# Kernel optimization log

Measured on AMD Instinct MI355X. Metric: run time of the kernel, lower is better.

Reference implementation:

```python
import jax, jax.numpy as jnp
import numpy as np

N_HEADS = 8
WINDOW = 4
KS = 3
N_LAYERS = 6
EPS = 1e-5


def _rel_to_abs(x):
    # x: [B,H,L,2L-1] relative logits -> [B,H,L,L] absolute
    b, h, l, _ = x.shape
    x = jnp.pad(x, ((0, 0), (0, 0), (0, 0), (0, 1)))
    x = x.reshape(b, h, l * 2 * l)
    x = jnp.pad(x, ((0, 0), (0, 0), (0, l - 1)))
    return x.reshape(b, h, l + 1, 2 * l - 1)[:, :, :l, l - 1:]


def _abs_to_rel(x):
    # x: [B,H,L,L] -> [B,H,L,2L-1]
    b, h, l, _ = x.shape
    x = jnp.pad(x, ((0, 0), (0, 0), (0, 0), (0, l - 1)))
    x = x.reshape(b, h, l * (2 * l - 1))
    x = jnp.pad(x, ((0, 0), (0, 0), (l, 0)))
    return x.reshape(b, h, l, 2 * l)[:, :, :, 1:]


def _get_rel_emb(emb, t):
    # emb: [2*WINDOW+1, D] -> [2t-1, D]
    pad = max(t - (WINDOW + 1), 0)
    start = max((WINDOW + 1) - t, 0)
    emb = jnp.pad(emb, ((pad, pad), (0, 0)))
    return emb[start:start + 2 * t - 1]


def _layer_norm(x, g, b):
    # normalize over channel dim (axis 1) of [B,C,T]
    m = jnp.mean(x, axis=1, keepdims=True)
    v = jnp.mean((x - m) ** 2, axis=1, keepdims=True)
    return (x - m) * jax.lax.rsqrt(v + EPS) * g[None, :, None] + b[None, :, None]


def _attn(x, w, bvec, erk, erv, attn_mask):
    # x: [B,C,T]; w: [4,C,C] (q,k,v,o 1x1 convs); bvec: [4,C]
    B, C, T = x.shape
    kch = C // N_HEADS

    def proj(i):
        h = jnp.einsum('oc,bct->bot', w[i], x) + bvec[i][None, :, None]
        return h.reshape(B, N_HEADS, kch, T).transpose(0, 1, 3, 2)  # [B,H,T,D]

    q, k, v = proj(0), proj(1), proj(2)
    scale = np.float32(1.0 / np.sqrt(kch))
    scores = jnp.einsum('bhtd,bhsd->bhts', q * scale, k)
    kr = _get_rel_emb(erk, T)  # [2T-1, D]
    scores = scores + _rel_to_abs(jnp.einsum('bhtd,md->bhtm', q * scale, kr))
    scores = jnp.where(attn_mask == 0, jnp.float32(-1e4), scores)
    p = jax.nn.softmax(scores, axis=-1)
    out = jnp.einsum('bhts,bhsd->bhtd', p, v)
    vr = _get_rel_emb(erv, T)
    out = out + jnp.einsum('bhtm,md->bhtd', _abs_to_rel(p), vr)
    out = out.transpose(0, 1, 3, 2).reshape(B, C, T)
    return jnp.einsum('oc,bct->bot', w[3], out) + bvec[3][None, :, None]


def _conv1d_same(h, wt, bt):
    pad_l, pad_r = (KS - 1) // 2, KS // 2
    hp = jnp.pad(h, ((0, 0), (0, 0), (pad_l, pad_r)))
    y = jax.lax.conv_general_dilated(hp, wt, (1,), 'VALID',
                                     dimension_numbers=('NCH', 'OIH', 'NCH'))
    return y + bt[None, :, None]


def _ffn(x, mask, w1, b1, w2, b2):
    h = jax.nn.relu(_conv1d_same(x * mask, w1, b1))  # activation=None -> relu
    return _conv1d_same(h * mask, w2, b2) * mask


def reference(x, x_mask, attn_w, attn_b, erk, erv, ln1_g, ln1_b,
              ffn_w1, ffn_b1, ffn_w2, ffn_b2, ln2_g, ln2_b):
    attn_mask = x_mask[:, :, :, None] * x_mask[:, :, None, :]  # [B,1,T,T]
    x = x * x_mask
    for i in range(N_LAYERS):
        y = _attn(x, attn_w[i], attn_b[i], erk[i], erv[i], attn_mask)
        x = _layer_norm(x + y, ln1_g[i], ln1_b[i])
        y = _ffn(x, x_mask, ffn_w1[i], ffn_b1[i], ffn_w2[i], ffn_b2[i])
        x = _layer_norm(x + y, ln2_g[i], ln2_b[i])
    return x * x_mask


def setup_inputs() -> dict:
    B, C, T, F, L = 8, 512, 1024, 2048, N_LAYERS
    kch = C // N_HEADS
    key = jax.random.key(0)
    ks = jax.random.split(key, 8)
    std = 0.02
    return {
        'x': jax.random.normal(ks[0], (B, C, T), jnp.float32),
        'x_mask': jnp.ones((B, 1, T), jnp.float32),
        'attn_w': jax.random.normal(ks[1], (L, 4, C, C), jnp.float32) * std,
        'attn_b': jnp.zeros((L, 4, C), jnp.float32),
        'erk': jax.random.normal(ks[2], (L, 2 * WINDOW + 1, kch), jnp.float32) * (kch ** -0.5),
        'erv': jax.random.normal(ks[3], (L, 2 * WINDOW + 1, kch), jnp.float32) * (kch ** -0.5),
        'ln1_g': jnp.ones((L, C), jnp.float32),
        'ln1_b': jnp.zeros((L, C), jnp.float32),
        'ffn_w1': jax.random.normal(ks[4], (L, F, C, KS), jnp.float32) * std,
        'ffn_b1': jnp.zeros((L, F), jnp.float32),
        'ffn_w2': jax.random.normal(ks[5], (L, C, F, KS), jnp.float32) * std,
        'ffn_b2': jnp.zeros((L, C), jnp.float32),
        'ln2_g': jnp.ones((L, C), jnp.float32),
        'ln2_b': jnp.zeros((L, C), jnp.float32),
    }
```

## Files before the change

### kernel.cpp

```cpp
#include <hip/hip_runtime.h>

typedef __bf16 bf16_t;
typedef __bf16 bf16x8 __attribute__((ext_vector_type(8)));
typedef __bf16 bf16x4 __attribute__((ext_vector_type(4)));
typedef float  f32x4  __attribute__((ext_vector_type(4)));

#define AS1 __attribute__((address_space(1)))
#define AS3 __attribute__((address_space(3)))

#define CMAX 16.0f

template<int BM, int BN, int OUTMN, int CONV, int BIAS, int RELU, int MASK>
__global__ __launch_bounds__(256)
void gemm_nt(const bf16_t* __restrict__ A, const bf16_t* __restrict__ B,
             bf16_t* __restrict__ C, const float* __restrict__ bias,
             const float* __restrict__ mask, const bf16_t* __restrict__ zpage,
             int K, int lda, int ldb, int ldc, int CIN,
             long sAb, long sAh, long sBb, long sBh, long sCb, long sCh)
{
    constexpr int BK = 32;
    __shared__ bf16_t As[BM * BK];
    __shared__ bf16_t Bs[BN * BK];
    const int z = blockIdx.z;
    int tap0 = 0;
    if constexpr (CONV == 2) {
        tap0 = z;
        A += (long)tap0 * CIN;
    } else {
        A += (long)(z >> 3) * sAb + (long)(z & 7) * sAh;
        B += (long)(z >> 3) * sBb + (long)(z & 7) * sBh;
        C += (long)(z >> 3) * sCb + (long)(z & 7) * sCh;
    }
    const int m0 = blockIdx.y * BM;
    const int n0 = blockIdx.x * BN;
    const int tid = threadIdx.x;
    const int wid = tid >> 6, lane = tid & 63;
    constexpr int WM = BM / 2, WN = BN / 2;
    constexpr int FM = WM / 16, FN = WN / 16;
    const int wm = wid >> 1, wn = wid & 1;

    f32x4 acc[FM][FN] = {};

    constexpr int ACH = BM / 64;
    constexpr int BCH = BN / 64;
    const int rquad = lane >> 2;
    const int koff  = (lane & 3) * 8;

    int tap = 0, cc0 = 0;
    for (int k0 = 0; k0 < K; k0 += BK) {
        #pragma unroll
        for (int q = 0; q < ACH; ++q) {
            int ch  = wid * ACH + q;
            int row = ch * 16 + rquad;
            const bf16_t* src = A + (long)(m0 + row) * lda + (k0 + koff);
            __builtin_amdgcn_global_load_lds((const AS1 void*)src,
                                             (AS3 void*)(As + ch * 512), 16, 0, 0);
        }
        #pragma unroll
        for (int q = 0; q < BCH; ++q) {
            int ch  = wid * BCH + q;
            int row = ch * 16 + rquad;
            const bf16_t* src;
            if constexpr (CONV == 1) {
                int tl = (n0 & 1023) + row + tap - 1;
                src = ((unsigned)tl < 1024u)
                    ? B + (long)(n0 + row + tap - 1) * ldb + (cc0 + koff)
                    : zpage + koff;
            } else if constexpr (CONV == 2) {
                int tl = (n0 & 1023) + row + tap0 - 1;
                src = ((unsigned)tl < 1024u)
                    ? B + (long)(n0 + row + tap0 - 1) * ldb + (k0 + koff)
                    : zpage + koff;
            } else {
                src = B + (long)(n0 + row) * ldb + (k0 + koff);
            }
            __builtin_amdgcn_global_load_lds((const AS1 void*)src,
                                             (AS3 void*)(Bs + ch * 512), 16, 0, 0);
        }
        if constexpr (CONV == 1) { cc0 += BK; if (cc0 == CIN) { cc0 = 0; ++tap; } }
        __syncthreads();

        const bf16_t* Ab = As + (wm * WM + (lane & 15)) * BK + ((lane >> 4) * 8);
        const bf16_t* Bb = Bs + (wn * WN + (lane & 15)) * BK + ((lane >> 4) * 8);
        bf16x8 af[FM], bv[FN];
        #pragma unroll
        for (int i = 0; i < FM; ++i) af[i] = *(const bf16x8*)(Ab + i * 16 * BK);
        #pragma unroll
        for (int j = 0; j < FN; ++j) bv[j] = *(const bf16x8*)(Bb + j * 16 * BK);
        #pragma unroll
        for (int i = 0; i < FM; ++i)
            #pragma unroll
            for (int j = 0; j < FN; ++j)
                acc[i][j] = __builtin_amdgcn_mfma_f32_16x16x32_bf16(af[i], bv[j], acc[i][j], 0, 0, 0);
        __syncthreads();
    }

    const int mw = m0 + wm * WM, nw = n0 + wn * WN;
    #pragma unroll
    for (int i = 0; i < FM; ++i) {
        const int mb = mw + i * 16 + (lane >> 4) * 4;
        f32x4 bvv = {};
        if constexpr (BIAS) bvv = *(const f32x4*)(bias + mb);
        #pragma unroll
        for (int j = 0; j < FN; ++j) {
            const int nn = nw + j * 16 + (lane & 15);
            f32x4 v = acc[i][j];
            if constexpr (BIAS) v += bvv;
            if constexpr (RELU) {
                #pragma unroll
                for (int r = 0; r < 4; ++r) v[r] = fmaxf(v[r], 0.f);
            }
            if constexpr (MASK) v *= mask[nn];
            bf16x4 o;
            #pragma unroll
            for (int r = 0; r < 4; ++r) o[r] = (bf16_t)v[r];
            if constexpr (CONV == 2) {
                *(bf16x4*)(C + ((long)tap0 << 22) + (long)nn * 512 + mb) = o;
            } else if constexpr (OUTMN) {
                #pragma unroll
                for (int r = 0; r < 4; ++r) C[(long)(mb + r) * ldc + nn] = (bf16_t)v[r];
            } else {
                *(bf16x4*)(C + (long)nn * ldc + mb) = o;
            }
        }
    }
}

__global__ __launch_bounds__(256)
void rel_qk(const bf16_t* __restrict__ qk, const float* __restrict__ erk_l,
            float* __restrict__ R)
{
    int gw = blockIdx.x * 4 + (threadIdx.x >> 6);
    int z = gw >> 10, t = gw & 1023;
    int b = z >> 3, h = z & 7;
    int lane = threadIdx.x & 63;
    float qv = (float)qk[(long)(b * 1024 + t) * 1024 + h * 64 + lane];
    float r[9];
    #pragma unroll
    for (int j = 0; j < 9; ++j) r[j] = qv * erk_l[j * 64 + lane];
    #pragma unroll
    for (int o = 1; o < 64; o <<= 1)
        #pragma unroll
        for (int j = 0; j < 9; ++j) r[j] += __shfl_xor(r[j], o);
    if (lane == 0) {
        #pragma unroll
        for (int j = 0; j < 9; ++j) R[(long)gw * 9 + j] = r[j];
    }
}

__global__ __launch_bounds__(256)
void mask_bias(const float* __restrict__ mask, float* __restrict__ kb)
{
    int i = blockIdx.x * 256 + threadIdx.x;
    if (i < 8192) kb[i] = (mask[i] == 0.f) ? -1e4f : 0.f;
}

__global__ __launch_bounds__(256)
void flash_attn(const bf16_t* __restrict__ qk, const bf16_t* __restrict__ vt,
                const float* __restrict__ R, const float* __restrict__ kb,
                bf16_t* __restrict__ out, float* __restrict__ stats)
{
    __shared__ bf16_t P_lds[4 * 1024];
    const int w = threadIdx.x >> 6, lane = threadIdx.x & 63;
    const int hi = lane >> 4, li = lane & 15;
    const int bh = blockIdx.x, b = bh >> 3, h = bh & 7;
    const int q0 = blockIdx.y * 64 + w * 16;
    const long nbase = (long)b * 1024;
    char* pw = (char*)(P_lds + w * 1024);

    const bf16_t* qrow = qk + (nbase + q0 + li) * 1024 + h * 64 + hi * 8;
    bf16x8 aq0 = *(const bf16x8*)(qrow);
    bf16x8 aq1 = *(const bf16x8*)(qrow + 32);

    bf16x8 ones;
    #pragma unroll
    for (int e = 0; e < 8; ++e) ones[e] = (bf16_t)1.0f;

    f32x4 acc_o[4] = {};
    f32x4 acc_l = {};

    const bf16_t* kbase = qk + nbase * 1024 + 512 + h * 64 + hi * 8;
    const bf16_t* vbase = vt + (long)(h * 64 + li) * 8192 + nbase + hi * 8;
    const float* kbp = kb + b * 1024;

    bf16x8 kc[4][2], vv[4][2];
    #pragma unroll
    for (int j = 0; j < 4; ++j) {
        const bf16_t* kr = kbase + (long)(j * 16 + li) * 1024;
        kc[j][0] = *(const bf16x8*)kr;
        kc[j][1] = *(const bf16x8*)(kr + 32);
    }

    for (int it = 0; it < 16; ++it) {
        const int s0 = it * 64;
        #pragma unroll
        for (int j2 = 0; j2 < 4; ++j2) {
            const bf16_t* vr = vbase + (long)(j2 * 16) * 8192 + s0;
            vv[j2][0] = *(const bf16x8*)vr;
            vv[j2][1] = *(const bf16x8*)(vr + 32);
        }
        float kbv[4];
        #pragma unroll
        for (int j = 0; j < 4; ++j) kbv[j] = kbp[s0 + j * 16 + li];
        f32x4 sc[4];
        __builtin_amdgcn_s_setprio(1);
        #pragma unroll
        for (int j = 0; j < 4; ++j) {
            f32x4 a = {};
            a = __builtin_amdgcn_mfma_f32_16x16x32_bf16(aq0, kc[j][0], a, 0, 0, 0);
            a = __builtin_amdgcn_mfma_f32_16x16x32_bf16(aq1, kc[j][1], a, 0, 0, 0);
            sc[j] = a;
        }
        __builtin_amdgcn_s_setprio(0);
        const int s1 = (s0 + 64) & 1023;
        #pragma unroll
        for (int j = 0; j < 4; ++j) {
            const bf16_t* kr = kbase + (long)(s1 + j * 16 + li) * 1024;
            kc[j][0] = *(const bf16x8*)kr;
            kc[j][1] = *(const bf16x8*)(kr + 32);
        }
        #pragma unroll
        for (int j = 0; j < 4; ++j) {
            const int sb = s0 + j * 16;
            const bool near = (sb + 15 >= q0 - 4) && (sb <= q0 + 19);
            const int s_abs = sb + li;
            #pragma unroll
            for (int r = 0; r < 4; ++r) {
                const int q_abs = q0 + hi * 4 + r;
                float v = sc[j][r] + kbv[j];
                if (near) {
                    int jb = s_abs - q_abs + 4;
                    if ((unsigned)jb < 9u)
                        v += R[((long)bh * 1024 + q_abs) * 9 + jb];
                }
                sc[j][r] = __expf(v - CMAX);
            }
        }
        #pragma unroll
        for (int j = 0; j < 4; ++j)
            #pragma unroll
            for (int r = 0; r < 4; ++r) {
                int q = hi * 4 + r;
                int c = (j * 32 + li * 2) ^ ((q & 7) << 4);
                *(bf16_t*)(pw + q * 128 + c) = (bf16_t)sc[j][r];
            }
        asm volatile("s_waitcnt lgkmcnt(0)" ::: "memory");
        __builtin_amdgcn_s_setprio(1);
        #pragma unroll
        for (int half = 0; half < 2; ++half) {
            int cr = (half * 64 + hi * 16) ^ ((li & 7) << 4);
            bf16x8 pa = *(const bf16x8*)(pw + li * 128 + cr);
            #pragma unroll
            for (int j2 = 0; j2 < 4; ++j2)
                acc_o[j2] = __builtin_amdgcn_mfma_f32_16x16x32_bf16(pa, vv[j2][half], acc_o[j2], 0, 0, 0);
            acc_l = __builtin_amdgcn_mfma_f32_16x16x32_bf16(pa, ones, acc_l, 0, 0, 0);
        }
        __builtin_amdgcn_s_setprio(0);
    }

    #pragma unroll
    for (int r = 0; r < 4; ++r) {
        const float inv = 1.f / acc_l[r];
        const int q_abs = q0 + hi * 4 + r;
        #pragma unroll
        for (int j2 = 0; j2 < 4; ++j2) {
            const int d = j2 * 16 + li;
            out[(nbase + q_abs) * 512 + h * 64 + d] = (bf16_t)(acc_o[j2][r] * inv);
        }
        if (li == 0) {
            stats[2 * ((long)bh * 1024 + q_abs)]     = CMAX;
            stats[2 * ((long)bh * 1024 + q_abs) + 1] = acc_l[r];
        }
    }
}

__global__ __launch_bounds__(256)
void band_finish(const bf16_t* __restrict__ qk, const float* __restrict__ R,
                 const float* __restrict__ stats, const float* __restrict__ erv_l,
                 const float* __restrict__ kb, bf16_t* __restrict__ out)
{
    int gw = blockIdx.x * 4 + (threadIdx.x >> 6);
    int bh = gw >> 10, t = gw & 1023;
    int b = bh >> 3, h = bh & 7;
    int lane = threadIdx.x & 63;
    const long nb = (long)b * 1024;
    float qv = (float)qk[(nb + t) * 1024 + h * 64 + lane];
    float p[9];
    #pragma unroll
    for (int j = 0; j < 9; ++j) {
        int s = t + j - 4;
        float dot = 0.f;
        if ((unsigned)s < 1024u)
            dot = qv * (float)qk[(nb + s) * 1024 + 512 + h * 64 + lane];
        p[j] = dot;
    }
    #pragma unroll
    for (int o = 1; o < 64; o <<= 1)
        #pragma unroll
        for (int j = 0; j < 9; ++j) p[j] += __shfl_xor(p[j], o);
    float m = stats[2 * (long)gw], invl = 1.f / stats[2 * (long)gw + 1];
    #pragma unroll
    for (int j = 0; j < 9; ++j) {
        int s = t + j - 4;
        if ((unsigned)s < 1024u) {
            float sc = p[j] + R[(long)gw * 9 + j] + kb[b * 1024 + s];
            p[j] = __expf(sc - m) * invl;
        } else p[j] = 0.f;
    }
    long oidx = (nb + t) * 512 + h * 64 + lane;
    float v = (float)out[oidx];
    #pragma unroll
    for (int j = 0; j < 9; ++j) v += p[j] * erv_l[j * 64 + lane];
    out[oidx] = (bf16_t)v;
}

template<int MASKOUT>
__global__ __launch_bounds__(256)
void ln_residual(float* __restrict__ xres, const bf16_t* __restrict__ y,
                 bf16_t* __restrict__ xbf, const float* __restrict__ g,
                 const float* __restrict__ bvec, const float* __restrict__ mask)
{
    int gw = blockIdx.x * 4 + (threadIdx.x >> 6);
    int lane = threadIdx.x & 63;
    long base = (long)gw * 512 + lane * 8;
    f32x4 x0 = *(const f32x4*)(xres + base);
    f32x4 x1 = *(const f32x4*)(xres + base + 4);
    bf16x8 yv = *(const bf16x8*)(y + base);
    float s[8];
    #pragma unroll
    for (int e = 0; e < 4; ++e) { s[e] = x0[e] + (float)yv[e]; s[4 + e] = x1[e] + (float)yv[4 + e]; }
    float sum = 0.f, sq = 0.f;
    #pragma unroll
    for (int e = 0; e < 8; ++e) { sum += s[e]; sq += s[e] * s[e]; }
    #pragma unroll
    for (int o = 1; o < 64; o <<= 1) { sum += __shfl_xor(sum, o); sq += __shfl_xor(sq, o); }
    float mean = sum * (1.f / 512.f);
    float var  = sq * (1.f / 512.f) - mean * mean;
    float rstd = rsqrtf(var + 1e-5f);
    f32x4 g0 = *(const f32x4*)(g + lane * 8);
    f32x4 g1 = *(const f32x4*)(g + lane * 8 + 4);
    f32x4 b0 = *(const f32x4*)(bvec + lane * 8);
    f32x4 b1 = *(const f32x4*)(bvec + lane * 8 + 4);
    float mk = MASKOUT ? mask[gw] : 1.f;
    f32x4 o0, o1; bf16x8 ob;
    #pragma unroll
    for (int e = 0; e < 4; ++e) {
        float v0 = (s[e] - mean) * rstd * g0[e] + b0[e];
        float v1 = (s[4 + e] - mean) * rstd * g1[e] + b1[e];
        o0[e] = v0; o1[e] = v1;
        ob[e] = (bf16_t)(v0 * mk); ob[4 + e] = (bf16_t)(v1 * mk);
    }
    *(f32x4*)(xres + base) = o0;
    *(f32x4*)(xres + base + 4) = o1;
    *(bf16x8*)(xbf + base) = ob;
}

__global__ __launch_bounds__(256)
void ln_residual_p3(float* __restrict__ xres, const bf16_t* __restrict__ part,
                    bf16_t* __restrict__ xbf, const float* __restrict__ g,
                    const float* __restrict__ bvec, const float* __restrict__ bias,
                    const float* __restrict__ mask)
{
    int gw = blockIdx.x * 4 + (threadIdx.x >> 6);
    int lane = threadIdx.x & 63;
    long base = (long)gw * 512 + lane * 8;
    bf16x8 pa = *(const bf16x8*)(part + base);
    bf16x8 pbv = *(const bf16x8*)(part + base + (1l << 22));
    bf16x8 pc = *(const bf16x8*)(part + base + (2l << 22));
    f32x4 x0 = *(const f32x4*)(xres + base);
    f32x4 x1 = *(const f32x4*)(xres + base + 4);
    f32x4 bi0 = *(const f32x4*)(bias + lane * 8);
    f32x4 bi1 = *(const f32x4*)(bias + lane * 8 + 4);
    float mk = mask[gw];
    float s[8];
    #pragma unroll
    for (int e = 0; e < 4; ++e) {
        float y0 = ((float)pa[e] + (float)pbv[e] + (float)pc[e] + bi0[e]) * mk;
        float y1 = ((float)pa[4 + e] + (float)pbv[4 + e] + (float)pc[4 + e] + bi1[e]) * mk;
        s[e] = x0[e] + y0; s[4 + e] = x1[e] + y1;
    }
    float sum = 0.f, sq = 0.f;
    #pragma unroll
    for (int e = 0; e < 8; ++e) { sum += s[e]; sq += s[e] * s[e]; }
    #pragma unroll
    for (int o = 1; o < 64; o <<= 1) { sum += __shfl_xor(sum, o); sq += __shfl_xor(sq, o); }
    float mean = sum * (1.f / 512.f);
    float var  = sq * (1.f / 512.f) - mean * mean;
    float rstd = rsqrtf(var + 1e-5f);
    f32x4 g0 = *(const f32x4*)(g + lane * 8);
    f32x4 g1 = *(const f32x4*)(g + lane * 8 + 4);
    f32x4 b0 = *(const f32x4*)(bvec + lane * 8);
    f32x4 b1 = *(const f32x4*)(bvec + lane * 8 + 4);
    f32x4 o0, o1; bf16x8 ob;
    #pragma unroll
    for (int e = 0; e < 4; ++e) {
        float v0 = (s[e] - mean) * rstd * g0[e] + b0[e];
        float v1 = (s[4 + e] - mean) * rstd * g1[e] + b1[e];
        o0[e] = v0; o1[e] = v1;
        ob[e] = (bf16_t)v0; ob[4 + e] = (bf16_t)v1;
    }
    *(f32x4*)(xres + base) = o0;
    *(f32x4*)(xres + base + 4) = o1;
    *(bf16x8*)(xbf + base) = ob;
}

__global__ __launch_bounds__(256)
void transpose_in_k(const float* __restrict__ x, const float* __restrict__ mask,
                    float* __restrict__ xres, bf16_t* __restrict__ xbf)
{
    __shared__ float tile[32][33];
    int b = blockIdx.z, c0 = blockIdx.y * 32, t0 = blockIdx.x * 32;
    int tx = threadIdx.x & 31, ty = threadIdx.x >> 5;
    #pragma unroll
    for (int r = 0; r < 4; ++r) {
        int cl = ty + r * 8;
        tile[cl][tx] = x[((long)b * 512 + c0 + cl) * 1024 + t0 + tx];
    }
    __syncthreads();
    #pragma unroll
    for (int r = 0; r < 4; ++r) {
        int tl = ty + r * 8;
        int n = b * 1024 + t0 + tl;
        float v = tile[tx][tl] * mask[n];
        xres[(long)n * 512 + c0 + tx] = v;
        xbf[(long)n * 512 + c0 + tx] = (bf16_t)v;
    }
}

__global__ __launch_bounds__(256)
void transpose_out_k(const float* __restrict__ xres, const float* __restrict__ mask,
                     float* __restrict__ out)
{
    __shared__ float tile[32][33];
    int b = blockIdx.z, c0 = blockIdx.y * 32, t0 = blockIdx.x * 32;
    int tx = threadIdx.x & 31, ty = threadIdx.x >> 5;
    #pragma unroll
    for (int r = 0; r < 4; ++r) {
        int tl = ty + r * 8;
        int n = b * 1024 + t0 + tl;
        tile[tl][tx] = xres[(long)n * 512 + c0 + tx] * mask[n];
    }
    __syncthreads();
    #pragma unroll
    for (int r = 0; r < 4; ++r) {
        int cl = ty + r * 8;
        out[((long)b * 512 + c0 + cl) * 1024 + t0 + tx] = tile[tx][cl];
    }
}

__global__ __launch_bounds__(256)
void pack_attn_w(const float* __restrict__ w, bf16_t* __restrict__ Wqk,
                 bf16_t* __restrict__ Wv, bf16_t* __restrict__ Wo)
{
    int idx = blockIdx.x * 256 + threadIdx.x;
    if (idx >= 4 * 512 * 512) return;
    int c = idx & 511;
    int o = (idx >> 9) & 511;
    int which = idx >> 18;
    float v = w[idx];
    if (which == 0) v *= 0.125f;
    if (which <= 1)      Wqk[(which * 512 + o) * 512 + c] = (bf16_t)v;
    else if (which == 2) Wv[o * 512 + c] = (bf16_t)v;
    else                 Wo[o * 512 + c] = (bf16_t)v;
}

__global__ __launch_bounds__(256)
void pack_attn_b(const float* __restrict__ bsrc, float* __restrict__ bqk)
{
    int idx = blockIdx.x * 256 + threadIdx.x;
    if (idx >= 6 * 2 * 512) return;
    int c = idx & 511, which = (idx >> 9) & 1, i = idx >> 10;
    float v = bsrc[(i * 4 + which) * 512 + c];
    if (which == 0) v *= 0.125f;
    bqk[i * 1024 + which * 512 + c] = v;
}

__global__ __launch_bounds__(256)
void pack_w1k(const float* __restrict__ w, bf16_t* __restrict__ Wp)
{
    int idx = blockIdx.x * 256 + threadIdx.x;
    if (idx >= 2048 * 1536) return;
    int c = idx & 511;
    int k = (idx >> 9) % 3;
    int f = idx / 1536;
    Wp[idx] = (bf16_t)w[(f * 512 + c) * 3 + k];
}

__global__ __launch_bounds__(256)
void pack_w2k(const float* __restrict__ w, bf16_t* __restrict__ Wp)
{
    int idx = blockIdx.x * 256 + threadIdx.x;
    if (idx >= 512 * 6144) return;
    int f = idx & 2047;
    int k = (idx >> 11) % 3;
    int ci = idx / 6144;
    Wp[idx] = (bf16_t)w[ci * 6144 + f * 3 + k];
}

extern "C" void kernel_launch(void* const* d_in, const int* in_sizes, int n_in,
                              void* d_out, int out_size, void* d_ws, size_t ws_size,
                              hipStream_t stream)
{
    const float* x      = (const float*)d_in[0];
    const float* xmask  = (const float*)d_in[1];
    const float* attn_w = (const float*)d_in[2];
    const float* attn_b = (const float*)d_in[3];
    const float* erk    = (const float*)d_in[4];
    const float* erv    = (const float*)d_in[5];
    const float* ln1g   = (const float*)d_in[6];
    const float* ln1b   = (const float*)d_in[7];
    const float* w1     = (const float*)d_in[8];
    const float* b1in   = (const float*)d_in[9];
    const float* w2     = (const float*)d_in[10];
    const float* b2in   = (const float*)d_in[11];
    const float* ln2g   = (const float*)d_in[12];
    const float* ln2b   = (const float*)d_in[13];
    float* out = (float*)d_out;

    char* p = (char*)d_ws;
    auto alloc = [&](size_t bytes) {
        char* r = p;
        p += (bytes + 255) & ~(size_t)255;
        return r;
    };
    bf16_t* zpage = (bf16_t*)alloc(1024);
    bf16_t* Wqk_l = (bf16_t*)alloc(1024l * 512 * 2);
    bf16_t* Wv_l  = (bf16_t*)alloc(512l * 512 * 2);
    bf16_t* Wo_l  = (bf16_t*)alloc(512l * 512 * 2);
    bf16_t* W1p_l = (bf16_t*)alloc(2048l * 1536 * 2);
    bf16_t* W2p_l = (bf16_t*)alloc(512l * 6144 * 2);
    float*  bqk   = (float*)alloc(6l * 1024 * 4);
    float*  xres  = (float*)alloc(8192l * 512 * 4);
    bf16_t* xbf   = (bf16_t*)alloc(8192l * 512 * 2);
    bf16_t* big   = (bf16_t*)alloc(8192l * 2048 * 2);
    bf16_t* ybuf  = (bf16_t*)alloc(8192l * 512 * 2);
    bf16_t* part  = (bf16_t*)alloc(3l * 8192 * 512 * 2);
    float*  R     = (float*)alloc(64l * 1024 * 9 * 4);
    float*  stats = (float*)alloc(64l * 1024 * 2 * 4);
    float*  kb    = (float*)alloc(8192l * 4);
    (void)in_sizes; (void)n_in; (void)out_size; (void)ws_size;

    bf16_t* qk       = big;
    bf16_t* vt       = big + 8192l * 1024;
    bf16_t* attn_out = vt + 512l * 8192;
    bf16_t* hbuf     = big;

    hipMemsetAsync(zpage, 0, 1024, stream);
    pack_attn_b<<<24, 256, 0, stream>>>(attn_b, bqk);
    mask_bias<<<32, 256, 0, stream>>>(xmask, kb);
    transpose_in_k<<<dim3(32, 16, 8), 256, 0, stream>>>(x, xmask, xres, xbf);

    for (int i = 0; i < 6; ++i) {
        pack_attn_w<<<4096, 256, 0, stream>>>(attn_w + (long)i * 4 * 512 * 512,
                                              Wqk_l, Wv_l, Wo_l);
        pack_w1k<<<12288, 256, 0, stream>>>(w1 + (long)i * 2048 * 512 * 3, W1p_l);
        pack_w2k<<<12288, 256, 0, stream>>>(w2 + (long)i * 512 * 2048 * 3, W2p_l);

        gemm_nt<128, 128, 0, 0, 1, 0, 0><<<dim3(64, 8, 1), 256, 0, stream>>>(
            Wqk_l, xbf, qk, bqk + i * 1024, nullptr, zpage,
            512, 512, 512, 1024, 0, 0, 0, 0, 0, 0, 0);
        gemm_nt<64, 128, 1, 0, 1, 0, 0><<<dim3(64, 8, 1), 256, 0, stream>>>(
            Wv_l, xbf, vt, attn_b + (i * 4 + 2) * 512, nullptr, zpage,
            512, 512, 512, 8192, 0, 0, 0, 0, 0, 0, 0);
        rel_qk<<<16384, 256, 0, stream>>>(qk, erk + i * 576, R);
        flash_attn<<<dim3(64, 16), 256, 0, stream>>>(qk, vt, R, kb,
                                                     attn_out, stats);
        band_finish<<<16384, 256, 0, stream>>>(qk, R, stats, erv + i * 576,
                                               kb, attn_out);
        gemm_nt<64, 128, 0, 0, 1, 0, 0><<<dim3(64, 8, 1), 256, 0, stream>>>(
            Wo_l, attn_out, ybuf, attn_b + (i * 4 + 3) * 512, nullptr, zpage,
            512, 512, 512, 512, 0, 0, 0, 0, 0, 0, 0);
        ln_residual<1><<<2048, 256, 0, stream>>>(xres, ybuf, xbf,
                                                 ln1g + i * 512, ln1b + i * 512, xmask);
        gemm_nt<128, 128, 0, 1, 1, 1, 1><<<dim3(64, 16, 1), 256, 0, stream>>>(
            W1p_l, xbf, hbuf, b1in + i * 2048, xmask, zpage,
            1536, 1536, 512, 2048, 512, 0, 0, 0, 0, 0, 0);
        gemm_nt<64, 128, 0, 2, 0, 0, 0><<<dim3(64, 8, 3), 256, 0, stream>>>(
            W2p_l, hbuf, part, nullptr, nullptr, zpage,
            2048, 6144, 2048, 512, 2048, 0, 0, 0, 0, 0, 0);
        ln_residual_p3<<<2048, 256, 0, stream>>>(xres, part, xbf,
                                                 ln2g + i * 512, ln2b + i * 512,
                                                 b2in + i * 512, xmask);
    }

    transpose_out_k<<<dim3(32, 16, 8), 256, 0, stream>>>(xres, xmask, out);
}
```

Before: 2.890 ms.

## Turn FFN convolutions into plain GEMMs over overlapping rows with edge correction

Both kernel-size-3 FFN convolutions now run as ordinary GEMMs. The B operand is offset by one row, so each output reads three consecutive input rows as one contiguous K=3C vector. Where that window crosses a batch boundary, a small fix_edges kernel subtracts the wrong neighbour's contribution, and zeroed guard regions around the buffers cover the outer ends. This drops the per-tap bounds checks and the zero-page redirects from the GEMM inner loop, and the second FFN GEMM no longer splits into three tap partials that a separate reduction had to combine. In exchange, ReLU and masking move into an extra full pass over the 8192x2048 hidden buffer, and the second GEMM launches fewer blocks with a longer K loop.

```diff
diff --git a/kernel.cpp b/kernel.cpp
--- a/kernel.cpp
+++ b/kernel.cpp
@@ -10,27 +10,21 @@
 
 #define CMAX 16.0f
 
-template<int BM, int BN, int OUTMN, int CONV, int BIAS, int RELU, int MASK>
+template<int BM, int BN, int OUTMN, int BIAS, int RELU, int MASK>
 __global__ __launch_bounds__(256)
 void gemm_nt(const bf16_t* __restrict__ A, const bf16_t* __restrict__ B,
              bf16_t* __restrict__ C, const float* __restrict__ bias,
-             const float* __restrict__ mask, const bf16_t* __restrict__ zpage,
-             int K, int lda, int ldb, int ldc, int CIN,
+             const float* __restrict__ mask,
+             int K, int lda, int ldb, int ldc,
              long sAb, long sAh, long sBb, long sBh, long sCb, long sCh)
 {
     constexpr int BK = 32;
     __shared__ bf16_t As[BM * BK];
     __shared__ bf16_t Bs[BN * BK];
     const int z = blockIdx.z;
-    int tap0 = 0;
-    if constexpr (CONV == 2) {
-        tap0 = z;
-        A += (long)tap0 * CIN;
-    } else {
-        A += (long)(z >> 3) * sAb + (long)(z & 7) * sAh;
-        B += (long)(z >> 3) * sBb + (long)(z & 7) * sBh;
-        C += (long)(z >> 3) * sCb + (long)(z & 7) * sCh;
-    }
+    A += (long)(z >> 3) * sAb + (long)(z & 7) * sAh;
+    B += (long)(z >> 3) * sBb + (long)(z & 7) * sBh;
+    C += (long)(z >> 3) * sCb + (long)(z & 7) * sCh;
     const int m0 = blockIdx.y * BM;
     const int n0 = blockIdx.x * BN;
     const int tid = threadIdx.x;
@@ -46,7 +40,6 @@
     const int rquad = lane >> 2;
     const int koff  = (lane & 3) * 8;
 
-    int tap = 0, cc0 = 0;
     for (int k0 = 0; k0 < K; k0 += BK) {
         #pragma unroll
         for (int q = 0; q < ACH; ++q) {
@@ -60,24 +53,10 @@
         for (int q = 0; q < BCH; ++q) {
             int ch  = wid * BCH + q;
             int row = ch * 16 + rquad;
-            const bf16_t* src;
-            if constexpr (CONV == 1) {
-                int tl = (n0 & 1023) + row + tap - 1;
-                src = ((unsigned)tl < 1024u)
-                    ? B + (long)(n0 + row + tap - 1) * ldb + (cc0 + koff)
-                    : zpage + koff;
-            } else if constexpr (CONV == 2) {
-                int tl = (n0 & 1023) + row + tap0 - 1;
-                src = ((unsigned)tl < 1024u)
-                    ? B + (long)(n0 + row + tap0 - 1) * ldb + (k0 + koff)
-                    : zpage + koff;
-            } else {
-                src = B + (long)(n0 + row) * ldb + (k0 + koff);
-            }
+            const bf16_t* src = B + (long)(n0 + row) * ldb + (k0 + koff);
             __builtin_amdgcn_global_load_lds((const AS1 void*)src,
                                              (AS3 void*)(Bs + ch * 512), 16, 0, 0);
         }
-        if constexpr (CONV == 1) { cc0 += BK; if (cc0 == CIN) { cc0 = 0; ++tap; } }
         __syncthreads();
 
         const bf16_t* Ab = As + (wm * WM + (lane & 15)) * BK + ((lane >> 4) * 8);
@@ -111,19 +90,53 @@
                 for (int r = 0; r < 4; ++r) v[r] = fmaxf(v[r], 0.f);
             }
             if constexpr (MASK) v *= mask[nn];
-            bf16x4 o;
-            #pragma unroll
-            for (int r = 0; r < 4; ++r) o[r] = (bf16_t)v[r];
-            if constexpr (CONV == 2) {
-                *(bf16x4*)(C + ((long)tap0 << 22) + (long)nn * 512 + mb) = o;
-            } else if constexpr (OUTMN) {
+            if constexpr (OUTMN) {
                 #pragma unroll
                 for (int r = 0; r < 4; ++r) C[(long)(mb + r) * ldc + nn] = (bf16_t)v[r];
             } else {
+                bf16x4 o;
+                #pragma unroll
+                for (int r = 0; r < 4; ++r) o[r] = (bf16_t)v[r];
                 *(bf16x4*)(C + (long)nn * ldc + mb) = o;
             }
         }
     }
+}
+
+__global__ __launch_bounds__(256)
+void fix_edges(bf16_t* __restrict__ y, const bf16_t* __restrict__ W,
+               const bf16_t* __restrict__ x, const float* __restrict__ mask,
+               int F, int C, int useMask)
+{
+    int e = blockIdx.y, b = e >> 1, odd = e & 1;
+    long n = (long)b * 1024 + (odd ? 1023 : 0);
+    long xr = odd ? n + 1 : n - 1;
+    int tap = odd ? 2 : 0;
+    int f = blockIdx.x * 256 + threadIdx.x;
+    const bf16_t* wrow = W + ((long)f * 3 + tap) * C;
+    const bf16_t* xrow = x + xr * C;
+    float dot = 0.f;
+    for (int c = 0; c < C; c += 8) {
+        bf16x8 wv = *(const bf16x8*)(wrow + c);
+        bf16x8 xv = *(const bf16x8*)(xrow + c);
+        #pragma unroll
+        for (int k = 0; k < 8; ++k) dot += (float)wv[k] * (float)xv[k];
+    }
+    if (useMask) dot *= mask[n];
+    long idx = n * F + f;
+    y[idx] = (bf16_t)((float)y[idx] - dot);
+}
+
+__global__ __launch_bounds__(256)
+void relu_mask_k(bf16_t* __restrict__ h, const float* __restrict__ mask)
+{
+    int row = blockIdx.x;
+    float mk = mask[row];
+    bf16_t* hr = h + (long)row * 2048 + threadIdx.x * 8;
+    bf16x8 v = *(const bf16x8*)hr;
+    #pragma unroll
+    for (int k = 0; k < 8; ++k) v[k] = (bf16_t)(fmaxf((float)v[k], 0.f) * mk);
+    *(bf16x8*)hr = v;
 }
 
 __global__ __launch_bounds__(256)
@@ -356,55 +369,6 @@
 }
 
 __global__ __launch_bounds__(256)
-void ln_residual_p3(float* __restrict__ xres, const bf16_t* __restrict__ part,
-                    bf16_t* __restrict__ xbf, const float* __restrict__ g,
-                    const float* __restrict__ bvec, const float* __restrict__ bias,
-                    const float* __restrict__ mask)
-{
-    int gw = blockIdx.x * 4 + (threadIdx.x >> 6);
-    int lane = threadIdx.x & 63;
-    long base = (long)gw * 512 + lane * 8;
-    bf16x8 pa = *(const bf16x8*)(part + base);
-    bf16x8 pbv = *(const bf16x8*)(part + base + (1l << 22));
-    bf16x8 pc = *(const bf16x8*)(part + base + (2l << 22));
-    f32x4 x0 = *(const f32x4*)(xres + base);
-    f32x4 x1 = *(const f32x4*)(xres + base + 4);
-    f32x4 bi0 = *(const f32x4*)(bias + lane * 8);
-    f32x4 bi1 = *(const f32x4*)(bias + lane * 8 + 4);
-    float mk = mask[gw];
-    float s[8];
-    #pragma unroll
-    for (int e = 0; e < 4; ++e) {
-        float y0 = ((float)pa[e] + (float)pbv[e] + (float)pc[e] + bi0[e]) * mk;
-        float y1 = ((float)pa[4 + e] + (float)pbv[4 + e] + (float)pc[4 + e] + bi1[e]) * mk;
-        s[e] = x0[e] + y0; s[4 + e] = x1[e] + y1;
-    }
-    float sum = 0.f, sq = 0.f;
-    #pragma unroll
-    for (int e = 0; e < 8; ++e) { sum += s[e]; sq += s[e] * s[e]; }
-    #pragma unroll
-    for (int o = 1; o < 64; o <<= 1) { sum += __shfl_xor(sum, o); sq += __shfl_xor(sq, o); }
-    float mean = sum * (1.f / 512.f);
-    float var  = sq * (1.f / 512.f) - mean * mean;
-    float rstd = rsqrtf(var + 1e-5f);
-    f32x4 g0 = *(const f32x4*)(g + lane * 8);
-    f32x4 g1 = *(const f32x4*)(g + lane * 8 + 4);
-    f32x4 b0 = *(const f32x4*)(bvec + lane * 8);
-    f32x4 b1 = *(const f32x4*)(bvec + lane * 8 + 4);
-    f32x4 o0, o1; bf16x8 ob;
-    #pragma unroll
-    for (int e = 0; e < 4; ++e) {
-        float v0 = (s[e] - mean) * rstd * g0[e] + b0[e];
-        float v1 = (s[4 + e] - mean) * rstd * g1[e] + b1[e];
-        o0[e] = v0; o1[e] = v1;
-        ob[e] = (bf16_t)v0; ob[4 + e] = (bf16_t)v1;
-    }
-    *(f32x4*)(xres + base) = o0;
-    *(f32x4*)(xres + base + 4) = o1;
-    *(bf16x8*)(xbf + base) = ob;
-}
-
-__global__ __launch_bounds__(256)
 void transpose_in_k(const float* __restrict__ x, const float* __restrict__ mask,
                     float* __restrict__ xres, bf16_t* __restrict__ xbf)
 {
@@ -523,21 +487,22 @@
         p += (bytes + 255) & ~(size_t)255;
         return r;
     };
-    bf16_t* zpage = (bf16_t*)alloc(1024);
-    bf16_t* Wqk_l = (bf16_t*)alloc(1024l * 512 * 2);
-    bf16_t* Wv_l  = (bf16_t*)alloc(512l * 512 * 2);
-    bf16_t* Wo_l  = (bf16_t*)alloc(512l * 512 * 2);
-    bf16_t* W1p_l = (bf16_t*)alloc(2048l * 1536 * 2);
-    bf16_t* W2p_l = (bf16_t*)alloc(512l * 6144 * 2);
-    float*  bqk   = (float*)alloc(6l * 1024 * 4);
-    float*  xres  = (float*)alloc(8192l * 512 * 4);
-    bf16_t* xbf   = (bf16_t*)alloc(8192l * 512 * 2);
-    bf16_t* big   = (bf16_t*)alloc(8192l * 2048 * 2);
-    bf16_t* ybuf  = (bf16_t*)alloc(8192l * 512 * 2);
-    bf16_t* part  = (bf16_t*)alloc(3l * 8192 * 512 * 2);
-    float*  R     = (float*)alloc(64l * 1024 * 9 * 4);
-    float*  stats = (float*)alloc(64l * 1024 * 2 * 4);
-    float*  kb    = (float*)alloc(8192l * 4);
+    bf16_t* Wqk_l  = (bf16_t*)alloc(1024l * 512 * 2);
+    bf16_t* Wv_l   = (bf16_t*)alloc(512l * 512 * 2);
+    bf16_t* Wo_l   = (bf16_t*)alloc(512l * 512 * 2);
+    bf16_t* W1p_l  = (bf16_t*)alloc(2048l * 1536 * 2);
+    bf16_t* W2p_l  = (bf16_t*)alloc(512l * 6144 * 2);
+    float*  bqk    = (float*)alloc(6l * 1024 * 4);
+    float*  xres   = (float*)alloc(8192l * 512 * 4);
+    char*   guardA = alloc(1024);
+    bf16_t* xbf    = (bf16_t*)alloc(8192l * 512 * 2);
+    char*   guardB = alloc(4096);
+    bf16_t* big    = (bf16_t*)alloc(8192l * 2048 * 2);
+    char*   guardC = alloc(4096);
+    bf16_t* ybuf   = (bf16_t*)alloc(8192l * 512 * 2);
+    float*  R      = (float*)alloc(64l * 1024 * 9 * 4);
+    float*  stats  = (float*)alloc(64l * 1024 * 2 * 4);
+    float*  kb     = (float*)alloc(8192l * 4);
     (void)in_sizes; (void)n_in; (void)out_size; (void)ws_size;
 
     bf16_t* qk       = big;
@@ -545,7 +510,9 @@
     bf16_t* attn_out = vt + 512l * 8192;
     bf16_t* hbuf     = big;
 
-    hipMemsetAsync(zpage, 0, 1024, stream);
+    hipMemsetAsync(guardA, 0, 1024, stream);
+    hipMemsetAsync(guardB, 0, 4096, stream);
+    hipMemsetAsync(guardC, 0, 4096, stream);
     pack_attn_b<<<24, 256, 0, stream>>>(attn_b, bqk);
     mask_bias<<<32, 256, 0, stream>>>(xmask, kb);
     transpose_in_k<<<dim3(32, 16, 8), 256, 0, stream>>>(x, xmask, xres, xbf);
@@ -556,31 +523,35 @@
         pack_w1k<<<12288, 256, 0, stream>>>(w1 + (long)i * 2048 * 512 * 3, W1p_l);
         pack_w2k<<<12288, 256, 0, stream>>>(w2 + (long)i * 512 * 2048 * 3, W2p_l);
 
-        gemm_nt<128, 128, 0, 0, 1, 0, 0><<<dim3(64, 8, 1), 256, 0, stream>>>(
-            Wqk_l, xbf, qk, bqk + i * 1024, nullptr, zpage,
-            512, 512, 512, 1024, 0, 0, 0, 0, 0, 0, 0);
-        gemm_nt<64, 128, 1, 0, 1, 0, 0><<<dim3(64, 8, 1), 256, 0, stream>>>(
-            Wv_l, xbf, vt, attn_b + (i * 4 + 2) * 512, nullptr, zpage,
-            512, 512, 512, 8192, 0, 0, 0, 0, 0, 0, 0);
+        gemm_nt<128, 128, 0, 1, 0, 0><<<dim3(64, 8, 1), 256, 0, stream>>>(
+            Wqk_l, xbf, qk, bqk + i * 1024, nullptr,
+            512, 512, 512, 1024, 0, 0, 0, 0, 0, 0);
+        gemm_nt<64, 128, 1, 1, 0, 0><<<dim3(64, 8, 1), 256, 0, stream>>>(
+            Wv_l, xbf, vt, attn_b + (i * 4 + 2) * 512, nullptr,
+            512, 512, 512, 8192, 0, 0, 0, 0, 0, 0);
         rel_qk<<<16384, 256, 0, stream>>>(qk, erk + i * 576, R);
         flash_attn<<<dim3(64, 16), 256, 0, stream>>>(qk, vt, R, kb,
                                                      attn_out, stats);
         band_finish<<<16384, 256, 0, stream>>>(qk, R, stats, erv + i * 576,
                                                kb, attn_out);
-        gemm_nt<64, 128, 0, 0, 1, 0, 0><<<dim3(64, 8, 1), 256, 0, stream>>>(
-            Wo_l, attn_out, ybuf, attn_b + (i * 4 + 3) * 512, nullptr, zpage,
-            512, 512, 512, 512, 0, 0, 0, 0, 0, 0, 0);
+        gemm_nt<64, 128, 0, 1, 0, 0><<<dim3(64, 8, 1), 256, 0, stream>>>(
+            Wo_l, attn_out, ybuf, attn_b + (i * 4 + 3) * 512, nullptr,
+            512, 512, 512, 512, 0, 0, 0, 0, 0, 0);
         ln_residual<1><<<2048, 256, 0, stream>>>(xres, ybuf, xbf,
                                                  ln1g + i * 512, ln1b + i * 512, xmask);
-        gemm_nt<128, 128, 0, 1, 1, 1, 1><<<dim3(64, 16, 1), 256, 0, stream>>>(
-            W1p_l, xbf, hbuf, b1in + i * 2048, xmask, zpage,
-            1536, 1536, 512, 2048, 512, 0, 0, 0, 0, 0, 0);
-        gemm_nt<64, 128, 0, 2, 0, 0, 0><<<dim3(64, 8, 3), 256, 0, stream>>>(
-            W2p_l, hbuf, part, nullptr, nullptr, zpage,
-            2048, 6144, 2048, 512, 2048, 0, 0, 0, 0, 0, 0);
-        ln_residual_p3<<<2048, 256, 0, stream>>>(xres, part, xbf,
-                                                 ln2g + i * 512, ln2b + i * 512,
-                                                 b2in + i * 512, xmask);
+        gemm_nt<128, 128, 0, 1, 0, 0><<<dim3(64, 16, 1), 256, 0, stream>>>(
+            W1p_l, xbf - 512, hbuf, b1in + i * 2048, nullptr,
+            1536, 1536, 512, 2048, 0, 0, 0, 0, 0, 0);
+        fix_edges<<<dim3(8, 16), 256, 0, stream>>>(hbuf, W1p_l, xbf, nullptr,
+                                                   2048, 512, 0);
+        relu_mask_k<<<8192, 256, 0, stream>>>(hbuf, xmask);
+        gemm_nt<64, 128, 0, 1, 0, 1><<<dim3(64, 8, 1), 256, 0, stream>>>(
+            W2p_l, hbuf - 2048, ybuf, b2in + i * 512, xmask,
+            6144, 6144, 2048, 512, 0, 0, 0, 0, 0, 0);
+        fix_edges<<<dim3(2, 16), 256, 0, stream>>>(ybuf, W2p_l, hbuf, xmask,
+                                                   512, 2048, 1);
+        ln_residual<0><<<2048, 256, 0, stream>>>(xres, ybuf, xbf,
+                                                 ln2g + i * 512, ln2b + i * 512, xmask);
     }
 
     transpose_out_k<<<dim3(32, 16, 8), 256, 0, stream>>>(xres, xmask, out);
```

New measurement: 3.450 ms. 1.19x slower.

## Split attention key range across warps and combine partial sums in LDS

Applied to the files above, without the earlier changes.

Each flash_attn block now covers 32 query rows instead of 64. Its four warps are arranged as two query halves times two key halves of 512 keys each. The grid doubles to 64x32 blocks, and the two key-half partial outputs and row sums are merged through a shared-memory buffer after a block barrier. This is meant to raise parallelism and occupancy, since there were only 1024 blocks each looping over all 1024 keys. In exchange it adds a __syncthreads, about 8KB more LDS, and loads every query row twice across blocks.

```diff
diff --git a/kernel.cpp b/kernel.cpp
--- a/kernel.cpp
+++ b/kernel.cpp
@@ -161,10 +161,13 @@
                 bf16_t* __restrict__ out, float* __restrict__ stats)
 {
     __shared__ bf16_t P_lds[4 * 1024];
+    __shared__ float combo[2][1040];
     const int w = threadIdx.x >> 6, lane = threadIdx.x & 63;
     const int hi = lane >> 4, li = lane & 15;
     const int bh = blockIdx.x, b = bh >> 3, h = bh & 7;
-    const int q0 = blockIdx.y * 64 + w * 16;
+    const int qh = w & 1, sh = w >> 1;
+    const int q0 = blockIdx.y * 32 + qh * 16;
+    const int sbeg = sh * 512;
     const long nbase = (long)b * 1024;
     char* pw = (char*)(P_lds + w * 1024);
 
@@ -186,13 +189,13 @@
     bf16x8 kc[4][2], vv[4][2];
     #pragma unroll
     for (int j = 0; j < 4; ++j) {
-        const bf16_t* kr = kbase + (long)(j * 16 + li) * 1024;
+        const bf16_t* kr = kbase + (long)(sbeg + j * 16 + li) * 1024;
         kc[j][0] = *(const bf16x8*)kr;
         kc[j][1] = *(const bf16x8*)(kr + 32);
     }
 
-    for (int it = 0; it < 16; ++it) {
-        const int s0 = it * 64;
+    for (int it = 0; it < 8; ++it) {
+        const int s0 = sbeg + it * 64;
         #pragma unroll
         for (int j2 = 0; j2 < 4; ++j2) {
             const bf16_t* vr = vbase + (long)(j2 * 16) * 8192 + s0;
@@ -212,7 +215,7 @@
             sc[j] = a;
         }
         __builtin_amdgcn_s_setprio(0);
-        const int s1 = (s0 + 64) & 1023;
+        const int s1 = sbeg + ((it + 1) & 7) * 64;
         #pragma unroll
         for (int j = 0; j < 4; ++j) {
             const bf16_t* kr = kbase + (long)(s1 + j * 16 + li) * 1024;
@@ -258,18 +261,33 @@
         __builtin_amdgcn_s_setprio(0);
     }
 
-    #pragma unroll
-    for (int r = 0; r < 4; ++r) {
-        const float inv = 1.f / acc_l[r];
-        const int q_abs = q0 + hi * 4 + r;
-        #pragma unroll
-        for (int j2 = 0; j2 < 4; ++j2) {
-            const int d = j2 * 16 + li;
-            out[(nbase + q_abs) * 512 + h * 64 + d] = (bf16_t)(acc_o[j2][r] * inv);
-        }
-        if (li == 0) {
-            stats[2 * ((long)bh * 1024 + q_abs)]     = CMAX;
-            stats[2 * ((long)bh * 1024 + q_abs) + 1] = acc_l[r];
+    if (sh == 0) {
+        #pragma unroll
+        for (int r = 0; r < 4; ++r) {
+            int row = hi * 4 + r;
+            #pragma unroll
+            for (int j2 = 0; j2 < 4; ++j2)
+                combo[qh][row * 64 + j2 * 16 + li] = acc_o[j2][r];
+            if (li == 0) combo[qh][1024 + row] = acc_l[r];
+        }
+    }
+    __syncthreads();
+    if (sh == 1) {
+        #pragma unroll
+        for (int r = 0; r < 4; ++r) {
+            int row = hi * 4 + r;
+            float l = acc_l[r] + combo[qh][1024 + row];
+            float inv = 1.f / l;
+            int q_abs = q0 + row;
+            #pragma unroll
+            for (int j2 = 0; j2 < 4; ++j2) {
+                float v = acc_o[j2][r] + combo[qh][row * 64 + j2 * 16 + li];
+                out[(nbase + q_abs) * 512 + h * 64 + j2 * 16 + li] = (bf16_t)(v * inv);
+            }
+            if (li == 0) {
+                stats[2 * ((long)bh * 1024 + q_abs)]     = CMAX;
+                stats[2 * ((long)bh * 1024 + q_abs) + 1] = l;
+            }
         }
     }
 }
@@ -563,7 +581,7 @@
             Wv_l, xbf, vt, attn_b + (i * 4 + 2) * 512, nullptr, zpage,
             512, 512, 512, 8192, 0, 0, 0, 0, 0, 0, 0);
         rel_qk<<<16384, 256, 0, stream>>>(qk, erk + i * 576, R);
-        flash_attn<<<dim3(64, 16), 256, 0, stream>>>(qk, vt, R, kb,
+        flash_attn<<<dim3(64, 32), 256, 0, stream>>>(qk, vt, R, kb,
                                                      attn_out, stats);
         band_finish<<<16384, 256, 0, stream>>>(qk, R, stats, erv + i * 576,
                                                kb, attn_out);
```

Measured after the change: 2.932 ms. No clear change (+1.5%).

## Fuse relative-value band term into flash attention and drop band_finish kernel

Applied to the files above, without the earlier changes.

Flash attention now accumulates the nine banded softmax numerators per query row in registers while it computes exponentials. After a cross-lane reduction it applies the erv relative-value embedding before normalizing and writing the output. This removes the separate band_finish kernel, which recomputed QK dot products and reread the output, plus its stats buffer. It also adds a launch bound asking for 4 blocks per SIMD occupancy. The cost is extra registers and per-element compare logic in the inner loop, and register pressure under the new launch bound could cause spills.

```diff
diff --git a/kernel.cpp b/kernel.cpp
--- a/kernel.cpp
+++ b/kernel.cpp
@@ -155,10 +155,10 @@
     if (i < 8192) kb[i] = (mask[i] == 0.f) ? -1e4f : 0.f;
 }
 
-__global__ __launch_bounds__(256)
+__global__ __launch_bounds__(256, 4)
 void flash_attn(const bf16_t* __restrict__ qk, const bf16_t* __restrict__ vt,
                 const float* __restrict__ R, const float* __restrict__ kb,
-                bf16_t* __restrict__ out, float* __restrict__ stats)
+                const float* __restrict__ erv_l, bf16_t* __restrict__ out)
 {
     __shared__ bf16_t P_lds[4 * 1024];
     const int w = threadIdx.x >> 6, lane = threadIdx.x & 63;
@@ -178,6 +178,7 @@
 
     f32x4 acc_o[4] = {};
     f32x4 acc_l = {};
+    float pb[4][9] = {};
 
     const bf16_t* kbase = qk + nbase * 1024 + 512 + h * 64 + hi * 8;
     const bf16_t* vbase = vt + (long)(h * 64 + li) * 8192 + nbase + hi * 8;
@@ -233,7 +234,14 @@
                     if ((unsigned)jb < 9u)
                         v += R[((long)bh * 1024 + q_abs) * 9 + jb];
                 }
-                sc[j][r] = __expf(v - CMAX);
+                float pex = __expf(v - CMAX);
+                sc[j][r] = pex;
+                if (near) {
+                    const int jb = s_abs - q_abs + 4;
+                    #pragma unroll
+                    for (int jbc = 0; jbc < 9; ++jbc)
+                        if (jbc == jb) pb[r][jbc] += pex;
+                }
             }
         }
         #pragma unroll
@@ -259,59 +267,26 @@
     }
 
     #pragma unroll
+    for (int o = 1; o < 16; o <<= 1)
+        #pragma unroll
+        for (int r = 0; r < 4; ++r)
+            #pragma unroll
+            for (int jb = 0; jb < 9; ++jb)
+                pb[r][jb] += __shfl_xor(pb[r][jb], o);
+
+    #pragma unroll
     for (int r = 0; r < 4; ++r) {
         const float inv = 1.f / acc_l[r];
         const int q_abs = q0 + hi * 4 + r;
         #pragma unroll
         for (int j2 = 0; j2 < 4; ++j2) {
             const int d = j2 * 16 + li;
-            out[(nbase + q_abs) * 512 + h * 64 + d] = (bf16_t)(acc_o[j2][r] * inv);
-        }
-        if (li == 0) {
-            stats[2 * ((long)bh * 1024 + q_abs)]     = CMAX;
-            stats[2 * ((long)bh * 1024 + q_abs) + 1] = acc_l[r];
-        }
-    }
-}
-
-__global__ __launch_bounds__(256)
-void band_finish(const bf16_t* __restrict__ qk, const float* __restrict__ R,
-                 const float* __restrict__ stats, const float* __restrict__ erv_l,
-                 const float* __restrict__ kb, bf16_t* __restrict__ out)
-{
-    int gw = blockIdx.x * 4 + (threadIdx.x >> 6);
-    int bh = gw >> 10, t = gw & 1023;
-    int b = bh >> 3, h = bh & 7;
-    int lane = threadIdx.x & 63;
-    const long nb = (long)b * 1024;
-    float qv = (float)qk[(nb + t) * 1024 + h * 64 + lane];
-    float p[9];
-    #pragma unroll
-    for (int j = 0; j < 9; ++j) {
-        int s = t + j - 4;
-        float dot = 0.f;
-        if ((unsigned)s < 1024u)
-            dot = qv * (float)qk[(nb + s) * 1024 + 512 + h * 64 + lane];
-        p[j] = dot;
-    }
-    #pragma unroll
-    for (int o = 1; o < 64; o <<= 1)
-        #pragma unroll
-        for (int j = 0; j < 9; ++j) p[j] += __shfl_xor(p[j], o);
-    float m = stats[2 * (long)gw], invl = 1.f / stats[2 * (long)gw + 1];
-    #pragma unroll
-    for (int j = 0; j < 9; ++j) {
-        int s = t + j - 4;
-        if ((unsigned)s < 1024u) {
-            float sc = p[j] + R[(long)gw * 9 + j] + kb[b * 1024 + s];
-            p[j] = __expf(sc - m) * invl;
-        } else p[j] = 0.f;
-    }
-    long oidx = (nb + t) * 512 + h * 64 + lane;
-    float v = (float)out[oidx];
-    #pragma unroll
-    for (int j = 0; j < 9; ++j) v += p[j] * erv_l[j * 64 + lane];
-    out[oidx] = (bf16_t)v;
+            float v = acc_o[j2][r];
+            #pragma unroll
+            for (int jb = 0; jb < 9; ++jb) v += pb[r][jb] * erv_l[jb * 64 + d];
+            out[(nbase + q_abs) * 512 + h * 64 + d] = (bf16_t)(v * inv);
+        }
+    }
 }
 
 template<int MASKOUT>
@@ -536,7 +511,6 @@
     bf16_t* ybuf  = (bf16_t*)alloc(8192l * 512 * 2);
     bf16_t* part  = (bf16_t*)alloc(3l * 8192 * 512 * 2);
     float*  R     = (float*)alloc(64l * 1024 * 9 * 4);
-    float*  stats = (float*)alloc(64l * 1024 * 2 * 4);
     float*  kb    = (float*)alloc(8192l * 4);
     (void)in_sizes; (void)n_in; (void)out_size; (void)ws_size;
 
@@ -564,9 +538,7 @@
             512, 512, 512, 8192, 0, 0, 0, 0, 0, 0, 0);
         rel_qk<<<16384, 256, 0, stream>>>(qk, erk + i * 576, R);
         flash_attn<<<dim3(64, 16), 256, 0, stream>>>(qk, vt, R, kb,
-                                                     attn_out, stats);
-        band_finish<<<16384, 256, 0, stream>>>(qk, R, stats, erv + i * 576,
-                                               kb, attn_out);
+                                                     erv + i * 576, attn_out);
         gemm_nt<64, 128, 0, 0, 1, 0, 0><<<dim3(64, 8, 1), 256, 0, stream>>>(
             Wo_l, attn_out, ybuf, attn_b + (i * 4 + 3) * 512, nullptr, zpage,
             512, 512, 512, 512, 0, 0, 0, 0, 0, 0, 0);
```

Result: slower. 3.687 ms (+27.6%).
